# Kernel optimization log

Hardware: AMD Instinct MI355X
Metric: run time of the kernel (lower is better)

## Reference

```python
import jax, jax.numpy as jnp
import numpy as np

B, T, D, H, d = 2, 2048, 1024, 16, 64
INNER = H * d
SCALE = d ** -0.5


def _rope(x, inv_freq):
    # x: [B, H, T, d], interleaved rotary as in the torch module
    t = x.shape[2]
    pos = jnp.arange(t, dtype=jnp.float32)
    freqs = pos[:, None] * inv_freq[None, :]          # [T, d/2]
    cos_f, sin_f = jnp.cos(freqs), jnp.sin(freqs)
    x1, x2 = x[..., 0::2], x[..., 1::2]
    y1 = x1 * cos_f - x2 * sin_f
    y2 = x1 * sin_f + x2 * cos_f
    return jnp.stack([y1, y2], axis=-1).reshape(x.shape)


def setup_inputs() -> dict:
    key = jax.random.key(0)
    ks = jax.random.split(key, 6)
    x = jax.random.normal(ks[0], (B, T, D), jnp.float32)
    W_qkv = jax.random.normal(ks[1], (D, 3 * INNER), jnp.float32) * (D ** -0.5)
    W_out = jax.random.normal(ks[2], (INNER, D), jnp.float32) * (INNER ** -0.5)
    W_dt = jax.random.normal(ks[3], (D, H), jnp.float32) * 0.01
    b_dt = jnp.full((H,), -4.0, jnp.float32)
    W_gsp = jax.random.normal(ks[4], (D, INNER), jnp.float32) * 0.01
    b_gsp = jnp.full((INNER,), -3.0, jnp.float32)
    inv_freq = 1.0 / (10000.0 ** (jnp.arange(0, d, 2, dtype=jnp.float32) / d))
    return {"x": x, "W_qkv": W_qkv, "W_out": W_out, "W_dt": W_dt,
            "b_dt": b_dt, "W_gsp": W_gsp, "b_gsp": b_gsp, "inv_freq": inv_freq}


def reference(x, W_qkv, W_out, W_dt, b_dt, W_gsp, b_gsp, inv_freq):
    qkv = (x @ W_qkv).reshape(B, T, 3, H, d)
    Q = jnp.moveaxis(qkv[:, :, 0], 1, 2)   # [B,H,T,d]
    K = jnp.moveaxis(qkv[:, :, 1], 1, 2)
    V = jnp.moveaxis(qkv[:, :, 2], 1, 2)
    Q = _rope(Q, inv_freq)
    K = _rope(K, inv_freq)

    dt = jax.nn.softplus(x @ W_dt + b_dt)             # [B,T,H]
    gamma = jnp.moveaxis(jnp.exp(-dt), 1, 2)          # [B,H,T]

    p = jax.nn.sigmoid(x @ W_gsp + b_gsp).reshape(B, T, H, d)
    p = jnp.moveaxis(p, 1, 2)                          # [B,H,T,d]
    gamma_eff = gamma[..., None] * (1.0 - p) + p
    gamma_scalar = gamma_eff.mean(axis=-1)            # [B,H,T]
    V = V * (1.0 - p)

    log_gamma = jnp.log(jnp.clip(gamma_scalar, 1e-6, 1.0 - 1e-6))
    lgc = jnp.cumsum(log_gamma, axis=-1)              # [B,H,T]
    log_D = jnp.clip(lgc[..., :, None] - lgc[..., None, :], -20.0, 0.0)
    causal = jnp.tril(jnp.ones((T, T), jnp.float32))
    Dm = jnp.exp(log_D) * causal                      # [B,H,T,T]

    Wscore = jnp.einsum('bhtd,bhsd->bhts', Q * SCALE, K)
    A = Wscore * Dm
    Y = jnp.einsum('bhts,bhsd->bhtd', A, V)
    Y = jnp.moveaxis(Y, 1, 2).reshape(B, T, INNER)
    return Y @ W_out
```

## Files before the change

kernel.cpp:

```cpp
#include <hip/hip_runtime.h>
#include <hip/hip_bf16.h>
#include <math.h>

#define B_     2
#define T_     2048
#define D_     1024
#define H_     16
#define INNER_ 1024
#define NC_    4096
#define SCALE_ 0.125f

typedef unsigned short u16;
typedef short short8 __attribute__((ext_vector_type(8)));
typedef float f32x4 __attribute__((ext_vector_type(4)));
typedef float f32x16 __attribute__((ext_vector_type(16)));
typedef unsigned short u16x4 __attribute__((ext_vector_type(4)));

__device__ __forceinline__ u16 f2bf(float x) {
  union { float f; unsigned u; } v; v.f = x;
  unsigned r = v.u + 0x7fffu + ((v.u >> 16) & 1u);
  return (u16)(r >> 16);
}
__device__ __forceinline__ float b2f(u16 x) {
  union { unsigned u; float f; } v; v.u = ((unsigned)x) << 16;
  return v.f;
}
__device__ __forceinline__ void gload16(const void* g, void* l) {
  __builtin_amdgcn_global_load_lds(
      (const __attribute__((address_space(1))) void*)g,
      (__attribute__((address_space(3))) void*)l, 16, 0, 0);
}

__global__ __launch_bounds__(256) void prep_kernel(
    const float* __restrict__ x, const float* __restrict__ W_qkv,
    const float* __restrict__ W_gsp, const float* __restrict__ W_out,
    const float* __restrict__ W_dt, const float* __restrict__ inv_freq,
    u16* __restrict__ xb, u16* __restrict__ Wcombt, u16* __restrict__ Woutt,
    u16* __restrict__ Wdtb, float2* __restrict__ tab) {
  const int bid = blockIdx.x, tid = threadIdx.x;
  if (bid < 1280) {
    const float* src; u16* dst; int N, nx, ky;
    if (bid < 768)       { src = W_qkv; dst = Wcombt;                N = 3072; nx = bid % 48;          ky = bid / 48; }
    else if (bid < 1024) { src = W_gsp; dst = Wcombt + 3072 * 1024;  N = 1024; nx = (bid - 768) % 16;  ky = (bid - 768) / 16; }
    else                 { src = W_out; dst = Woutt;                 N = 1024; nx = (bid - 1024) % 16; ky = (bid - 1024) / 16; }
    __shared__ float tile[64][65];
    const int k0 = ky * 64, n0 = nx * 64;
    for (int e = tid; e < 4096; e += 256) {
      int kk = e >> 6, nn = e & 63;
      tile[kk][nn] = src[(size_t)(k0 + kk) * N + n0 + nn];
    }
    __syncthreads();
    for (int e = tid; e < 4096; e += 256) {
      int nn = e >> 6, kk = e & 63;
      dst[(size_t)(n0 + nn) * 1024 + k0 + kk] = f2bf(tile[kk][nn]);
    }
  } else if (bid < 1344) {
    int i = (bid - 1280) * 256 + tid;
    int k = i >> 4, h = i & 15;
    Wdtb[(size_t)h * D_ + k] = f2bf(W_dt[i]);
  } else if (bid < 1600) {
    int i = (bid - 1344) * 256 + tid;
    int t = i >> 5, j = i & 31;
    float s, c;
    sincosf((float)t * inv_freq[j], &s, &c);
    tab[i] = make_float2(c, s);
  } else {
    int base = (bid - 1600) * 1024 + tid;
#pragma unroll
    for (int r = 0; r < 4; ++r) {
      int i = base + r * 256;
      float4 v = *reinterpret_cast<const float4*>(x + (size_t)i * 4);
      u16x4 o; o.x = f2bf(v.x); o.y = f2bf(v.y); o.z = f2bf(v.z); o.w = f2bf(v.w);
      *reinterpret_cast<u16x4*>(xb + (size_t)i * 4) = o;
    }
  }
}

__global__ __launch_bounds__(256) void gamma_kernel(
    const u16* __restrict__ xb, const u16* __restrict__ Wdtb,
    const float* __restrict__ b_dt, float* __restrict__ gam) {
  const int row = blockIdx.x * 4 + (threadIdx.x >> 6);
  const int l = threadIdx.x & 63;
  const int h = l >> 2;
  const int kc = (l & 3) * 256;
  const short8* xp = (const short8*)(xb + (size_t)row * D_ + kc);
  const short8* wp = (const short8*)(Wdtb + h * D_ + kc);
  float s = 0.f;
#pragma unroll
  for (int i = 0; i < 32; ++i) {
    short8 xv = xp[i], wv = wp[i];
#pragma unroll
    for (int j = 0; j < 8; ++j) s += b2f((u16)xv[j]) * b2f((u16)wv[j]);
  }
  s += __shfl_xor(s, 1);
  s += __shfl_xor(s, 2);
  if ((l & 3) == 0) {
    float v = s + b_dt[h];
    float sp = (v > 20.f) ? v : log1pf(__expf(v));
    gam[row * H_ + h] = __expf(-sp);
  }
}

#define SWZG(r) ((((r) & 3) ^ (((r) >> 2) & 1)))

__device__ __forceinline__ void stage_op(const u16* __restrict__ gbase, int kt,
                                         char* ldst, int h, int tid) {
  int r = h * 128 + (tid >> 2);
  int kg = (tid & 3) ^ SWZG(r);
  gload16(gbase + (size_t)r * D_ + kt * 32 + kg * 8,
          ldst + (h * 128 + (tid >> 6) * 16) * 64);
}
__device__ __forceinline__ short8 ldfrag(const char* tile, int row, int g4) {
  return *(const short8*)(tile + row * 64 + ((g4 ^ SWZG(row)) << 4));
}

__global__ __launch_bounds__(512, 2) void gemm_big(
    const u16* __restrict__ A, const u16* __restrict__ Bt,
    u16* __restrict__ C) {
  __shared__ char lds[4 * 32768];
  const int tid = threadIdx.x;
  const int w = tid >> 6, l = tid & 63;
  const int bid = blockIdx.x;
  const int xcd = bid & 7, idx = bid >> 3;
  const int brow = (xcd >> 1) * 4 + (idx & 3);
  const int bcol = (xcd & 1) * 8 + (idx >> 2);
  const int m0 = brow * 256, n0 = bcol * 256;
  const int wr = (w >> 2) * 128, wc = (w & 3) * 64;
  const int ql = l & 15, g4 = l >> 4;

  const u16* Ag = A + (size_t)m0 * D_;
  const u16* Bg = Bt + (size_t)n0 * D_;

  f32x4 acc[8][4] = {};

#pragma unroll
  for (int t = 0; t < 3; ++t) {
    char* bufA = lds + t * 32768;
    char* bufB = bufA + 16384;
    stage_op(Ag, t, bufA, 0, tid); stage_op(Ag, t, bufA, 1, tid);
    stage_op(Bg, t, bufB, 0, tid); stage_op(Bg, t, bufB, 1, tid);
  }

  const int NT = D_ / 32;
  for (int kt = 0; kt < NT; ++kt) {
    if (kt < NT - 2)       asm volatile("s_waitcnt vmcnt(8)" ::: "memory");
    else if (kt == NT - 2) asm volatile("s_waitcnt vmcnt(4)" ::: "memory");
    else                   asm volatile("s_waitcnt vmcnt(0)" ::: "memory");
    __builtin_amdgcn_sched_barrier(0);
    __builtin_amdgcn_s_barrier();
    __builtin_amdgcn_sched_barrier(0);

    char* bufA = lds + (kt & 3) * 32768;
    char* bufB = bufA + 16384;
    char* nbufA = lds + ((kt + 3) & 3) * 32768;
    char* nbufB = nbufA + 16384;
    const bool pre = (kt + 3 < NT);

    if (pre) {
      stage_op(Ag, kt + 3, nbufA, 0, tid);
      stage_op(Ag, kt + 3, nbufA, 1, tid);
    }
    short8 bf[4];
#pragma unroll
    for (int nf = 0; nf < 4; ++nf) bf[nf] = ldfrag(bufB, wc + nf * 16 + ql, g4);
    short8 af[4];
#pragma unroll
    for (int mf = 0; mf < 4; ++mf) af[mf] = ldfrag(bufA, wr + mf * 16 + ql, g4);
    __builtin_amdgcn_s_setprio(1);
#pragma unroll
    for (int mf = 0; mf < 4; ++mf)
#pragma unroll
      for (int nf = 0; nf < 4; ++nf)
        acc[mf][nf] = __builtin_amdgcn_mfma_f32_16x16x32_bf16(af[mf], bf[nf], acc[mf][nf], 0, 0, 0);
    __builtin_amdgcn_s_setprio(0);

    if (pre) {
      stage_op(Bg, kt + 3, nbufB, 0, tid);
      stage_op(Bg, kt + 3, nbufB, 1, tid);
    }
    short8 af2[4];
#pragma unroll
    for (int mf = 0; mf < 4; ++mf) af2[mf] = ldfrag(bufA, wr + 64 + mf * 16 + ql, g4);
    __builtin_amdgcn_s_setprio(1);
#pragma unroll
    for (int mf = 0; mf < 4; ++mf)
#pragma unroll
      for (int nf = 0; nf < 4; ++nf)
        acc[mf + 4][nf] = __builtin_amdgcn_mfma_f32_16x16x32_bf16(af2[mf], bf[nf], acc[mf + 4][nf], 0, 0, 0);
    __builtin_amdgcn_s_setprio(0);
  }

#pragma unroll
  for (int mf = 0; mf < 8; ++mf) {
#pragma unroll
    for (int r = 0; r < 4; ++r) {
      size_t row = (size_t)(m0 + wr + mf * 16 + g4 * 4 + r);
      size_t base = row * NC_ + n0 + wc + ql;
#pragma unroll
      for (int nf = 0; nf < 4; ++nf)
        C[base + nf * 16] = f2bf(acc[mf][nf][r]);
    }
  }
}

template <bool BF16OUT>
__global__ __launch_bounds__(256) void gemm_bt(
    const u16* __restrict__ A, const u16* __restrict__ Bt,
    void* __restrict__ Cv, int M, int N, int K) {
  __shared__ u16 As[2][128 * 64] __attribute__((aligned(16)));
  __shared__ u16 Bs[2][128 * 64] __attribute__((aligned(16)));
  const int tid = threadIdx.x, w = tid >> 6, l = tid & 63;
  const int rpx = (M >> 7) >> 3;
  const int bid = blockIdx.x;
  const int xcd = bid & 7, idx = bid >> 3;
  const int brow = xcd * rpx + (idx % rpx);
  const int bcol = idx / rpx;
  const int m0 = brow * 128, n0 = bcol * 128;
  const int wr = (w >> 1) * 64, wc = (w & 1) * 64;
  const int srow = l >> 3;
  const int kgrp = ((l & 7) ^ srow) * 8;

  f32x4 acc[4][4] = {};

  auto stage = [&](int kt, int bs) {
#pragma unroll
    for (int i = 0; i < 4; ++i) {
      int c = w * 4 + i;
      int row = c * 8 + srow;
      gload16(A + (size_t)(m0 + row) * K + kt * 64 + kgrp, (char*)As[bs] + c * 1024);
      gload16(Bt + (size_t)(n0 + row) * K + kt * 64 + kgrp, (char*)Bs[bs] + c * 1024);
    }
  };

  stage(0, 0);
  const int NT = K >> 6;
  for (int kt = 0; kt < NT; ++kt) {
    if (kt + 1 < NT) {
      stage(kt + 1, (kt + 1) & 1);
      asm volatile("s_waitcnt vmcnt(8)" ::: "memory");
    } else {
      asm volatile("s_waitcnt vmcnt(0)" ::: "memory");
    }
    __builtin_amdgcn_sched_barrier(0);
    __builtin_amdgcn_s_barrier();
    __builtin_amdgcn_sched_barrier(0);
    const char* Asb = (const char*)As[kt & 1];
    const char* Bsb = (const char*)Bs[kt & 1];
#pragma unroll
    for (int kk = 0; kk < 2; ++kk) {
      short8 af[4], bf[4];
#pragma unroll
      for (int i = 0; i < 4; ++i) {
        int ra = wr + i * 16 + (l & 15);
        int sa = kk * 4 + (l >> 4);
        af[i] = *(const short8*)(Asb + ra * 128 + ((sa ^ (ra & 7)) << 4));
        int rb = wc + i * 16 + (l & 15);
        bf[i] = *(const short8*)(Bsb + rb * 128 + ((sa ^ (rb & 7)) << 4));
      }
#pragma unroll
      for (int i = 0; i < 4; ++i)
#pragma unroll
        for (int j = 0; j < 4; ++j)
          acc[i][j] = __builtin_amdgcn_mfma_f32_16x16x32_bf16(af[i], bf[j], acc[i][j], 0, 0, 0);
    }
    if (kt + 1 < NT) __builtin_amdgcn_s_barrier();
  }
#pragma unroll
  for (int i = 0; i < 4; ++i) {
#pragma unroll
    for (int r = 0; r < 4; ++r) {
      size_t row = (size_t)(m0 + wr + i * 16 + (l >> 4) * 4 + r);
      size_t base = row * N + n0 + wc + (l & 15);
#pragma unroll
      for (int j = 0; j < 4; ++j) {
        if (BF16OUT) ((u16*)Cv)[base + j * 16] = f2bf(acc[i][j][r]);
        else         ((float*)Cv)[base + j * 16] = acc[i][j][r];
      }
    }
  }
}

__global__ __launch_bounds__(256) void pointwise_kernel(
    const u16* __restrict__ C, const float* __restrict__ gam,
    const float* __restrict__ b_gsp, const float2* __restrict__ tab,
    u16* __restrict__ Qb, u16* __restrict__ Kb, u16* __restrict__ Vb,
    float* __restrict__ lg) {
  const int row = blockIdx.x * 4 + (threadIdx.x >> 6);
  const int l = threadIdx.x & 63;
  const int b = row >> 11, t = row & (T_ - 1);
  const int h = l >> 2;
  const int dd0 = (l & 3) * 16;
  const int col = h * 64 + dd0;
  const size_t cb = (size_t)row * NC_;

  const float gh = gam[row * H_ + h];
  const short8* qp = (const short8*)(C + cb + col);
  const short8* kp = (const short8*)(C + cb + 1024 + col);
  const short8* vp = (const short8*)(C + cb + 2048 + col);
  const short8* pp = (const short8*)(C + cb + 3072 + col);
  short8 q0 = qp[0], q1 = qp[1];
  short8 k0 = kp[0], k1 = kp[1];
  short8 v0 = vp[0], v1 = vp[1];
  short8 pr0 = pp[0], pr1 = pp[1];

  float ge = 0.f;
  short8 vo0, vo1;
#pragma unroll
  for (int i = 0; i < 8; ++i) {
    float pv = b2f((u16)pr0[i]) + b_gsp[col + i];
    float p = 1.f / (1.f + __expf(-pv));
    ge += gh * (1.f - p) + p;
    vo0[i] = (short)f2bf(b2f((u16)v0[i]) * (1.f - p));
    float pv1 = b2f((u16)pr1[i]) + b_gsp[col + 8 + i];
    float p1 = 1.f / (1.f + __expf(-pv1));
    ge += gh * (1.f - p1) + p1;
    vo1[i] = (short)f2bf(b2f((u16)v1[i]) * (1.f - p1));
  }
  const size_t hm = (((size_t)(b * H_ + h)) * T_ + t) * 64 + dd0;
  ((short8*)(Vb + hm))[0] = vo0;
  ((short8*)(Vb + hm))[1] = vo1;

  ge += __shfl_xor(ge, 1);
  ge += __shfl_xor(ge, 2);
  if ((l & 3) == 0) {
    float gs = ge * (1.f / 64.f);
    gs = fminf(fmaxf(gs, 1e-6f), 1.f - 1e-6f);
    lg[((size_t)(b * H_ + h)) * T_ + t] = logf(gs);
  }

  short8 qo0, qo1, ko0, ko1;
  const float2* cs = tab + t * 32 + (dd0 >> 1);
#pragma unroll
  for (int m = 0; m < 4; ++m) {
    float2 c0 = cs[m];
    float qa = b2f((u16)q0[2 * m]), qb = b2f((u16)q0[2 * m + 1]);
    qo0[2 * m]     = (short)f2bf((qa * c0.x - qb * c0.y) * SCALE_);
    qo0[2 * m + 1] = (short)f2bf((qa * c0.y + qb * c0.x) * SCALE_);
    float ka = b2f((u16)k0[2 * m]), kb = b2f((u16)k0[2 * m + 1]);
    ko0[2 * m]     = (short)f2bf(ka * c0.x - kb * c0.y);
    ko0[2 * m + 1] = (short)f2bf(ka * c0.y + kb * c0.x);
    float2 c1 = cs[4 + m];
    float qa1 = b2f((u16)q1[2 * m]), qb1 = b2f((u16)q1[2 * m + 1]);
    qo1[2 * m]     = (short)f2bf((qa1 * c1.x - qb1 * c1.y) * SCALE_);
    qo1[2 * m + 1] = (short)f2bf((qa1 * c1.y + qb1 * c1.x) * SCALE_);
    float ka1 = b2f((u16)k1[2 * m]), kb1 = b2f((u16)k1[2 * m + 1]);
    ko1[2 * m]     = (short)f2bf(ka1 * c1.x - kb1 * c1.y);
    ko1[2 * m + 1] = (short)f2bf(ka1 * c1.y + kb1 * c1.x);
  }
  ((short8*)(Qb + hm))[0] = qo0; ((short8*)(Qb + hm))[1] = qo1;
  ((short8*)(Kb + hm))[0] = ko0; ((short8*)(Kb + hm))[1] = ko1;
}

__global__ __launch_bounds__(256) void scan_kernel(
    const float* __restrict__ lg, float* __restrict__ lgc) {
  const size_t base = (size_t)blockIdx.x * T_;
  const int tid = threadIdx.x;
  __shared__ float sums[256];
  float loc[8];
  float run = 0.f;
#pragma unroll
  for (int i = 0; i < 8; ++i) { run += lg[base + tid * 8 + i]; loc[i] = run; }
  sums[tid] = run;
  __syncthreads();
  if (tid == 0) {
    float r = 0.f;
    for (int i = 0; i < 256; ++i) { float v = sums[i]; sums[i] = r; r += v; }
  }
  __syncthreads();
  const float off = sums[tid];
#pragma unroll
  for (int i = 0; i < 8; ++i) lgc[base + tid * 8 + i] = off + loc[i];
}

__global__ __launch_bounds__(256) void kv_prep_kernel(
    const u16* __restrict__ Vb, const float* __restrict__ lgc,
    u16* __restrict__ Vtg) {
  const int stile = blockIdx.x;
  const int bh = blockIdx.y;
  const int tid = threadIdx.x;
  __shared__ u16 vt[64][72];
  const size_t base = ((size_t)bh * T_ + (size_t)stile * 64) * 64;
  const float* lgp = lgc + (size_t)bh * T_;
  const float lgb = lgp[stile * 64];
#pragma unroll
  for (int i = 0; i < 2; ++i) {
    int c = tid * 2 + i;
    int row = c >> 3, k8 = (c & 7) * 8;
    float beta = __expf(lgb - lgp[stile * 64 + row]);
    short8 vv = *(const short8*)(Vb + base + row * 64 + k8);
#pragma unroll
    for (int j = 0; j < 8; ++j) vt[row][k8 + j] = f2bf(b2f((u16)vv[j]) * beta);
  }
  __syncthreads();
#pragma unroll
  for (int i = 0; i < 2; ++i) {
    int c = tid * 2 + i;
    int dd = c >> 3, t8 = (c & 7) * 8;
    short8 o;
#pragma unroll
    for (int j = 0; j < 8; ++j) o[j] = (short)vt[t8 + j][dd];
    *(short8*)(Vtg + ((size_t)(bh * 32 + stile) * 64 + dd) * 64 + t8) = o;
  }
}

__global__ __launch_bounds__(256) void attn_mfma(
    const u16* __restrict__ Qb, const u16* __restrict__ Kb,
    const u16* __restrict__ Vtg, const float* __restrict__ lgc,
    u16* __restrict__ Y) {
  const int i = blockIdx.x;
  const int xcd = i & 7;
  const int half = i >> 8;
  const int r = (i >> 3) & 31;
  const int q8 = r >> 2;
  const int bh_hi = r & 3;
  const int qb = half ? (15 - q8) : q8;
  const int bh = xcd + (bh_hi << 3);
  const int b = bh >> 4, h = bh & 15;
  const int tid = threadIdx.x, w = tid >> 6, l = tid & 63;
  const int l31 = l & 31, hi = l >> 5;
  __shared__ u16 Ks[4][64 * 64] __attribute__((aligned(16)));
  __shared__ u16 Vs[4][64 * 64] __attribute__((aligned(16)));
  __shared__ u16 Ps[4][2048] __attribute__((aligned(16)));
  const u16* Qg = Qb + (size_t)bh * T_ * 64;
  const u16* Kg = Kb + (size_t)bh * T_ * 64;
  const u16* Vg = Vtg + (size_t)bh * 32 * 4096;
  const float* lgp = lgc + (size_t)bh * T_;
  const int srow = l >> 3, slot8 = l & 7;

  const int q0 = qb * 128 + w * 32;
  const int qg = q0 + l31;
  short8 qf[4];
#pragma unroll
  for (int kk = 0; kk < 4; ++kk)
    qf[kk] = *(const short8*)(Qg + (size_t)qg * 64 + kk * 16 + hi * 8);
  const float lgq = lgp[qg];
  const float lgtop = lgp[qb * 128];

  char* Pw = (char*)Ps[w];
  const int psw = l31 & 7;

  f32x16 yacc0 = {}, yacc1 = {};

  const int st0 = qb * 2 + 1;
  int s_min;
  {
    int lo = 0, hic = st0;
    while (lo < hic) {
      int mid = (lo + hic) >> 1;
      if (lgtop - lgp[mid * 64 + 63] > -20.f) hic = mid; else lo = mid + 1;
    }
    s_min = lo;
  }

  auto STAGE = [&](int s) {
#pragma unroll
    for (int i2 = 0; i2 < 2; ++i2) {
      int c = w * 2 + i2, row = c * 8 + srow;
      int kg = (slot8 ^ (row & 7)) * 8;
      gload16(Kg + (size_t)(s * 64 + row) * 64 + kg, (char*)Ks[s & 3] + c * 1024);
      gload16(Vg + (size_t)s * 4096 + row * 64 + kg, (char*)Vs[s & 3] + c * 1024);
    }
  };

  STAGE(st0);
  if (st0 - 1 >= s_min) STAGE(st0 - 1);
  if (st0 - 2 >= s_min) STAGE(st0 - 2);

  for (int st = st0; st >= s_min; --st) {
    __builtin_amdgcn_s_barrier();
    if (st - 3 >= s_min) {
      STAGE(st - 3);
      asm volatile("s_waitcnt vmcnt(12)" ::: "memory");
    } else if (st - 2 >= s_min) {
      asm volatile("s_waitcnt vmcnt(8)" ::: "memory");
    } else if (st - 1 >= s_min) {
      asm volatile("s_waitcnt vmcnt(4)" ::: "memory");
    } else {
      asm volatile("s_waitcnt vmcnt(0)" ::: "memory");
    }
    __builtin_amdgcn_sched_barrier(0);

    const bool allinv = (st * 64 > q0 + 31);
    if (!allinv) {
      const char* Ksb = (const char*)Ks[st & 3];
      const char* Vsb = (const char*)Vs[st & 3];
      const float alpha = __expf(lgq - lgp[st * 64]);
      const bool domask = (st * 64 + 63 > q0);
      const int qrel = qg - st * 64;
#pragma unroll
      for (int sblk = 0; sblk < 2; ++sblk) {
        f32x16 c = {};
        __builtin_amdgcn_s_setprio(1);
#pragma unroll
        for (int kk = 0; kk < 4; ++kk) {
          int row = sblk * 32 + l31;
          short8 kf = *(const short8*)(Ksb + row * 128 + (((kk * 2 + hi) ^ (row & 7)) << 4));
          c = __builtin_amdgcn_mfma_f32_32x32x16_bf16(kf, qf[kk], c, 0, 0, 0);
        }
        __builtin_amdgcn_s_setprio(0);
#pragma unroll
        for (int bq = 0; bq < 4; ++bq) {
          u16x4 pk;
#pragma unroll
          for (int r2 = 0; r2 < 4; ++r2) {
            int s64 = sblk * 32 + bq * 8 + hi * 4 + r2;
            float pv = c[bq * 4 + r2] * alpha;
            if (domask && s64 > qrel) pv = 0.f;
            pk[r2] = f2bf(pv);
          }
          int slot = sblk * 4 + bq;
          *(u16x4*)(Pw + l31 * 128 + ((slot ^ psw) << 4) + hi * 8) = pk;
        }
      }
#pragma unroll
      for (int kk = 0; kk < 4; ++kk) {
        short8 pf = *(const short8*)(Pw + l31 * 128 + (((kk * 2 + hi) ^ psw) << 4));
        short8 vf0 = *(const short8*)(Vsb + l31 * 128 + (((kk * 2 + hi) ^ (l31 & 7)) << 4));
        short8 vf1 = *(const short8*)(Vsb + (32 + l31) * 128 + (((kk * 2 + hi) ^ (l31 & 7)) << 4));
        __builtin_amdgcn_s_setprio(1);
        yacc0 = __builtin_amdgcn_mfma_f32_32x32x16_bf16(pf, vf0, yacc0, 0, 0, 0);
        yacc1 = __builtin_amdgcn_mfma_f32_32x32x16_bf16(pf, vf1, yacc1, 0, 0, 0);
        __builtin_amdgcn_s_setprio(0);
      }
    }
  }

#pragma unroll
  for (int reg = 0; reg < 16; ++reg) {
    int qrow = (reg & 3) + 8 * (reg >> 2) + 4 * hi;
    size_t rowg = (size_t)(b * T_) + qb * 128 + w * 32 + qrow;
    Y[rowg * INNER_ + h * 64 + l31] = f2bf(yacc0[reg]);
    Y[rowg * INNER_ + h * 64 + 32 + l31] = f2bf(yacc1[reg]);
  }
}

extern "C" void kernel_launch(void* const* d_in, const int* in_sizes, int n_in,
                              void* d_out, int out_size, void* d_ws, size_t ws_size,
                              hipStream_t stream) {
  const float* x        = (const float*)d_in[0];
  const float* W_qkv    = (const float*)d_in[1];
  const float* W_out    = (const float*)d_in[2];
  const float* W_dt     = (const float*)d_in[3];
  const float* b_dt     = (const float*)d_in[4];
  const float* W_gsp    = (const float*)d_in[5];
  const float* b_gsp    = (const float*)d_in[6];
  const float* inv_freq = (const float*)d_in[7];
  float* out = (float*)d_out;

  const int M = B_ * T_;
  char* p = (char*)d_ws;
  auto alloc = [&](size_t bytes) {
    char* r = p; p += (bytes + 255) & ~(size_t)255; return r;
  };
  u16*    xb    = (u16*)alloc((size_t)M * D_ * 2);
  u16*    Wcombt= (u16*)alloc((size_t)NC_ * D_ * 2);
  u16*    Woutt = (u16*)alloc((size_t)D_ * INNER_ * 2);
  u16*    Wdtb  = (u16*)alloc((size_t)H_ * D_ * 2);
  u16*    Cqkvp = (u16*)alloc((size_t)M * NC_ * 2);
  u16*    Qb    = (u16*)alloc((size_t)B_ * H_ * T_ * 64 * 2);
  u16*    Kb    = (u16*)alloc((size_t)B_ * H_ * T_ * 64 * 2);
  u16*    Vb    = (u16*)alloc((size_t)B_ * H_ * T_ * 64 * 2);
  float*  gam   = (float*)alloc((size_t)M * H_ * 4);
  float*  lg    = (float*)alloc((size_t)B_ * H_ * T_ * 4);
  float*  lgc   = (float*)alloc((size_t)B_ * H_ * T_ * 4);
  float2* tab   = (float2*)alloc((size_t)T_ * 32 * 8);
  u16*    Vtg   = Cqkvp;
  u16*    Yb    = Cqkvp + (size_t)4 * 1024 * 1024;

  prep_kernel<<<2624, 256, 0, stream>>>(x, W_qkv, W_gsp, W_out, W_dt, inv_freq,
                                        xb, Wcombt, Woutt, Wdtb, tab);
  gamma_kernel<<<M / 4, 256, 0, stream>>>(xb, Wdtb, b_dt, gam);
  gemm_big<<<256, 512, 0, stream>>>(xb, Wcombt, Cqkvp);

  pointwise_kernel<<<M / 4, 256, 0, stream>>>(Cqkvp, gam, b_gsp, tab,
                                              Qb, Kb, Vb, lg);
  scan_kernel<<<B_ * H_, 256, 0, stream>>>(lg, lgc);
  kv_prep_kernel<<<dim3(T_ / 64, B_ * H_), 256, 0, stream>>>(Vb, lgc, Vtg);

  attn_mfma<<<512, 256, 0, stream>>>(Qb, Kb, Vtg, lgc, Yb);

  gemm_bt<false><<<256, 256, 0, stream>>>(Yb, Woutt, out, M, D_, INNER_);
}
```

Before: 156.1 us.

## Add GEMM LDS waits/barrier, shrink attention K/V ring to 3, use packed bf16 convert

In the GEMM main loop, explicit lgkmcnt(0) waits and scheduling barriers now sit before each MFMA burst, plus an extra workgroup barrier between the two halves, to control instruction ordering. The attention kernel cuts its K/V LDS ring from four stages to three (prefetch distance 2) to save LDS and possibly raise occupancy, with adjusted vmcnt waits. P conversion now uses the hardware v_cvt_pk_bf16_f32 instruction and splits the masked and unmasked paths. The extra barrier and shallower prefetch may expose more latency.

```diff
diff --git a/kernel.cpp b/kernel.cpp
--- a/kernel.cpp
+++ b/kernel.cpp
@@ -15,6 +15,7 @@
 typedef float f32x4 __attribute__((ext_vector_type(4)));
 typedef float f32x16 __attribute__((ext_vector_type(16)));
 typedef unsigned short u16x4 __attribute__((ext_vector_type(4)));
+typedef unsigned int u32x2 __attribute__((ext_vector_type(2)));
 
 __device__ __forceinline__ u16 f2bf(float x) {
   union { float f; unsigned u; } v; v.f = x;
@@ -24,6 +25,11 @@
 __device__ __forceinline__ float b2f(u16 x) {
   union { unsigned u; float f; } v; v.u = ((unsigned)x) << 16;
   return v.f;
+}
+__device__ __forceinline__ unsigned cvtpk(float lo, float hi) {
+  unsigned r;
+  asm("v_cvt_pk_bf16_f32 %0, %1, %2" : "=v"(r) : "v"(lo), "v"(hi));
+  return r;
 }
 __device__ __forceinline__ void gload16(const void* g, void* l) {
   __builtin_amdgcn_global_load_lds(
@@ -166,6 +172,8 @@
     short8 af[4];
 #pragma unroll
     for (int mf = 0; mf < 4; ++mf) af[mf] = ldfrag(bufA, wr + mf * 16 + ql, g4);
+    asm volatile("s_waitcnt lgkmcnt(0)" ::: "memory");
+    __builtin_amdgcn_sched_barrier(0);
     __builtin_amdgcn_s_setprio(1);
 #pragma unroll
     for (int mf = 0; mf < 4; ++mf)
@@ -173,6 +181,7 @@
       for (int nf = 0; nf < 4; ++nf)
         acc[mf][nf] = __builtin_amdgcn_mfma_f32_16x16x32_bf16(af[mf], bf[nf], acc[mf][nf], 0, 0, 0);
     __builtin_amdgcn_s_setprio(0);
+    __builtin_amdgcn_s_barrier();
 
     if (pre) {
       stage_op(Bg, kt + 3, nbufB, 0, tid);
@@ -181,6 +190,8 @@
     short8 af2[4];
 #pragma unroll
     for (int mf = 0; mf < 4; ++mf) af2[mf] = ldfrag(bufA, wr + 64 + mf * 16 + ql, g4);
+    asm volatile("s_waitcnt lgkmcnt(0)" ::: "memory");
+    __builtin_amdgcn_sched_barrier(0);
     __builtin_amdgcn_s_setprio(1);
 #pragma unroll
     for (int mf = 0; mf < 4; ++mf)
@@ -418,8 +429,8 @@
   const int b = bh >> 4, h = bh & 15;
   const int tid = threadIdx.x, w = tid >> 6, l = tid & 63;
   const int l31 = l & 31, hi = l >> 5;
-  __shared__ u16 Ks[4][64 * 64] __attribute__((aligned(16)));
-  __shared__ u16 Vs[4][64 * 64] __attribute__((aligned(16)));
+  __shared__ u16 Ks[3][64 * 64] __attribute__((aligned(16)));
+  __shared__ u16 Vs[3][64 * 64] __attribute__((aligned(16)));
   __shared__ u16 Ps[4][2048] __attribute__((aligned(16)));
   const u16* Qg = Qb + (size_t)bh * T_ * 64;
   const u16* Kg = Kb + (size_t)bh * T_ * 64;
@@ -453,25 +464,23 @@
   }
 
   auto STAGE = [&](int s) {
+    const int bs = s % 3;
 #pragma unroll
     for (int i2 = 0; i2 < 2; ++i2) {
       int c = w * 2 + i2, row = c * 8 + srow;
       int kg = (slot8 ^ (row & 7)) * 8;
-      gload16(Kg + (size_t)(s * 64 + row) * 64 + kg, (char*)Ks[s & 3] + c * 1024);
-      gload16(Vg + (size_t)s * 4096 + row * 64 + kg, (char*)Vs[s & 3] + c * 1024);
+      gload16(Kg + (size_t)(s * 64 + row) * 64 + kg, (char*)Ks[bs] + c * 1024);
+      gload16(Vg + (size_t)s * 4096 + row * 64 + kg, (char*)Vs[bs] + c * 1024);
     }
   };
 
   STAGE(st0);
   if (st0 - 1 >= s_min) STAGE(st0 - 1);
-  if (st0 - 2 >= s_min) STAGE(st0 - 2);
 
   for (int st = st0; st >= s_min; --st) {
     __builtin_amdgcn_s_barrier();
-    if (st - 3 >= s_min) {
-      STAGE(st - 3);
-      asm volatile("s_waitcnt vmcnt(12)" ::: "memory");
-    } else if (st - 2 >= s_min) {
+    if (st - 2 >= s_min) {
+      STAGE(st - 2);
       asm volatile("s_waitcnt vmcnt(8)" ::: "memory");
     } else if (st - 1 >= s_min) {
       asm volatile("s_waitcnt vmcnt(4)" ::: "memory");
@@ -482,8 +491,9 @@
 
     const bool allinv = (st * 64 > q0 + 31);
     if (!allinv) {
-      const char* Ksb = (const char*)Ks[st & 3];
-      const char* Vsb = (const char*)Vs[st & 3];
+      const int bs = st % 3;
+      const char* Ksb = (const char*)Ks[bs];
+      const char* Vsb = (const char*)Vs[bs];
       const float alpha = __expf(lgq - lgp[st * 64]);
       const bool domask = (st * 64 + 63 > q0);
       const int qrel = qg - st * 64;
@@ -498,18 +508,29 @@
           c = __builtin_amdgcn_mfma_f32_32x32x16_bf16(kf, qf[kk], c, 0, 0, 0);
         }
         __builtin_amdgcn_s_setprio(0);
-#pragma unroll
-        for (int bq = 0; bq < 4; ++bq) {
-          u16x4 pk;
-#pragma unroll
-          for (int r2 = 0; r2 < 4; ++r2) {
-            int s64 = sblk * 32 + bq * 8 + hi * 4 + r2;
-            float pv = c[bq * 4 + r2] * alpha;
-            if (domask && s64 > qrel) pv = 0.f;
-            pk[r2] = f2bf(pv);
+        if (domask) {
+#pragma unroll
+          for (int bq = 0; bq < 4; ++bq) {
+            float p0 = c[bq * 4 + 0] * alpha, p1 = c[bq * 4 + 1] * alpha;
+            float p2 = c[bq * 4 + 2] * alpha, p3 = c[bq * 4 + 3] * alpha;
+            int s64 = sblk * 32 + bq * 8 + hi * 4;
+            if (s64 + 0 > qrel) p0 = 0.f;
+            if (s64 + 1 > qrel) p1 = 0.f;
+            if (s64 + 2 > qrel) p2 = 0.f;
+            if (s64 + 3 > qrel) p3 = 0.f;
+            u32x2 pk; pk.x = cvtpk(p0, p1); pk.y = cvtpk(p2, p3);
+            int slot = sblk * 4 + bq;
+            *(u32x2*)(Pw + l31 * 128 + ((slot ^ psw) << 4) + hi * 8) = pk;
           }
-          int slot = sblk * 4 + bq;
-          *(u16x4*)(Pw + l31 * 128 + ((slot ^ psw) << 4) + hi * 8) = pk;
+        } else {
+#pragma unroll
+          for (int bq = 0; bq < 4; ++bq) {
+            u32x2 pk;
+            pk.x = cvtpk(c[bq * 4 + 0] * alpha, c[bq * 4 + 1] * alpha);
+            pk.y = cvtpk(c[bq * 4 + 2] * alpha, c[bq * 4 + 3] * alpha);
+            int slot = sblk * 4 + bq;
+            *(u32x2*)(Pw + l31 * 128 + ((slot ^ psw) << 4) + hi * 8) = pk;
+          }
         }
       }
 #pragma unroll
```

Measured after the change: 153.8 us. About the same (-1.4%).
